# Kernel optimization log

Hardware: AMD Instinct MI355X
Metric: run time of the kernel (lower is better)

The kernel has to match this reference:

```python
import jax, jax.numpy as jnp
import numpy as np

B, S, D, H, E, TOPK = 8, 1024, 512, 2048, 8, 2


def setup_inputs() -> dict:
    key = jax.random.key(0)
    ks = jax.random.split(key, 7)
    scale = 0.02
    return {
        "x": jax.random.normal(ks[0], (B, S, D), jnp.float32),
        "gate_w": jax.random.normal(ks[1], (D, E), jnp.float32) * scale,
        "gate_b": jnp.zeros((E,), jnp.float32),
        "w1": jax.random.normal(ks[2], (E, D, H), jnp.float32) * scale,
        "b1": jnp.zeros((E, H), jnp.float32),
        "w2": jax.random.normal(ks[3], (E, H, D), jnp.float32) * scale,
        "b2": jnp.zeros((E, D), jnp.float32),
    }


def reference(x, gate_w, gate_b, w1, b1, w2, b2):
    # ---- MoE transformer MLP (fastmoe FMoETransformerMLP, NaiveGate) ----
    xt = x.reshape(-1, D)                       # [T, D], T = B*S tokens
    logits = xt @ gate_w + gate_b               # [T, E]
    top_val, top_idx = jax.lax.top_k(logits, TOPK)  # [T, k]
    score = jax.nn.softmax(top_val, axis=-1)    # softmax over the k selected logits

    y = jnp.zeros_like(xt)
    # Loop over the small fixed expert set; each token's combine weight for
    # expert e is the sum of its top-k scores routed to e (0 if not selected).
    for e in range(E):
        w_tok = jnp.sum(score * (top_idx == e), axis=-1)        # [T]
        h = jax.nn.gelu(xt @ w1[e] + b1[e], approximate=False)  # [T, H]
        y = y + w_tok[:, None] * (h @ w2[e] + b2[e])            # [T, D]

    y = y.reshape(B, S, D)
    # Outer model: log_softmax over seq of channel-summed features
    return jax.nn.log_softmax(jnp.sum(y, axis=2), axis=1)       # [B, S]
```

## Files before the change

### kernel.cpp

```cpp
#include <hip/hip_runtime.h>
#include <hip/hip_bf16.h>
#include <math.h>

#define T_TOK 8192
#define DIM   512
#define NEXP  8
#define HID   2048
#define NBAT  8
#define SEQ   1024

typedef short  short8 __attribute__((ext_vector_type(8)));
typedef float  f32x4  __attribute__((ext_vector_type(4)));

__device__ __forceinline__ unsigned short f2bf(float f) {
    union { float f; unsigned int u; } v; v.f = f;
    unsigned int u = v.u;
    unsigned int r = u + 0x7FFFu + ((u >> 16) & 1u);
    return (unsigned short)(r >> 16);
}

__device__ __forceinline__ float gelu_f(float v) {
    float v2 = v * v;
    float w = v * (-2.302344f - 0.102955f * v2);
    return v / (1.f + __builtin_amdgcn_exp2f(w));
}

__global__ void prep_gate_k(const float* __restrict__ w1, unsigned short* __restrict__ w1f,
                            const float* __restrict__ w2, const float* __restrict__ b2,
                            float* __restrict__ w2sum, float* __restrict__ b2sum,
                            int* __restrict__ counts,
                            const float* __restrict__ x, const float* __restrict__ gw,
                            const float* __restrict__ gb,
                            unsigned short* __restrict__ xb,
                            int* __restrict__ eidx, float* __restrict__ esc0,
                            float* __restrict__ esc1) {
    int bid = blockIdx.x;
    int tid = threadIdx.x;
    int wave = tid >> 6, lane = tid & 63;
    if (bid < 2048) {
        __shared__ unsigned short tile[64][68];
        int e = bid >> 8, r = bid & 255;
        int d0 = (r & 7) * 64, h0 = (r >> 3) * 64;
        const float* src = w1 + (size_t)e * DIM * HID;
        #pragma unroll
        for (int pass = 0; pass < 4; ++pass) {
            int dr = pass * 16 + (tid >> 4);
            int hc = (tid & 15) * 4;
            float4 v = *(const float4*)(src + (size_t)(d0 + dr) * HID + h0 + hc);
            tile[hc + 0][dr] = f2bf(v.x);
            tile[hc + 1][dr] = f2bf(v.y);
            tile[hc + 2][dr] = f2bf(v.z);
            tile[hc + 3][dr] = f2bf(v.w);
        }
        __syncthreads();
        int l = tid & 63, q = l >> 4, c = l & 15;
        int kk0 = (r & 7) * 2, g0 = (r >> 3) * 4;
        #pragma unroll
        for (int pi = 0; pi < 2; ++pi) {
            int sub = pi * 4 + wave;
            int kk2 = sub >> 2, g2 = sub & 3;
            const unsigned short* tp = &tile[g2 * 16 + c][kk2 * 32 + q * 8];
            ushort4 a = *(const ushort4*)(tp);
            ushort4 b = *(const ushort4*)(tp + 4);
            unsigned short* dst = w1f +
                ((size_t)(e * 128 + g0 + g2) * 16 + kk0 + kk2) * 512 + l * 8;
            *(ushort4*)(dst)     = a;
            *(ushort4*)(dst + 4) = b;
        }
    } else if (bid < 4096) {
        int t = (bid - 2048) * 4 + wave;
        const float* xp = x + (size_t)t * DIM;
        unsigned short* xbp = xb + (size_t)t * DIM;
        float acc[8] = {0, 0, 0, 0, 0, 0, 0, 0};
        #pragma unroll
        for (int it = 0; it < 8; ++it) {
            int d = it * 64 + lane;
            float xv = xp[d];
            xbp[d] = f2bf(xv);
            float4 g0 = *(const float4*)(gw + d * 8);
            float4 g1 = *(const float4*)(gw + d * 8 + 4);
            acc[0] += xv * g0.x; acc[1] += xv * g0.y; acc[2] += xv * g0.z; acc[3] += xv * g0.w;
            acc[4] += xv * g1.x; acc[5] += xv * g1.y; acc[6] += xv * g1.z; acc[7] += xv * g1.w;
        }
        #pragma unroll
        for (int e = 0; e < 8; ++e) {
            float s = acc[e];
            #pragma unroll
            for (int off = 32; off >= 1; off >>= 1) s += __shfl_xor(s, off);
            acc[e] = s + gb[e];
        }
        float v0 = -1e30f, v1 = -1e30f; int i0 = 0, i1 = 0;
        #pragma unroll
        for (int e = 0; e < 8; ++e) {
            float v = acc[e];
            if (v > v0) { v1 = v0; i1 = i0; v0 = v; i0 = e; }
            else if (v > v1) { v1 = v; i1 = e; }
        }
        float e1 = expf(v1 - v0);
        float inv = 1.f / (1.f + e1);
        if (lane == 0) {
            eidx[t] = i0 | (i1 << 4);
            esc0[t] = inv;
            esc1[t] = e1 * inv;
        }
    } else if (bid < 8192) {
        int row = (bid - 4096) * 4 + wave;
        const float* p = w2 + (size_t)row * DIM;
        float4 a = *(const float4*)(p + lane * 4);
        float4 b = *(const float4*)(p + 256 + lane * 4);
        float s = a.x + a.y + a.z + a.w + b.x + b.y + b.z + b.w;
        #pragma unroll
        for (int off = 32; off >= 1; off >>= 1) s += __shfl_xor(s, off);
        if (lane == 0) w2sum[row] = s;
    } else {
        if (tid < 8) counts[tid] = 0;
        for (int r = wave; r < NEXP; r += 4) {
            const float* p = b2 + (size_t)r * DIM;
            float s = 0.f;
            for (int i = lane; i < DIM; i += 64) s += p[i];
            #pragma unroll
            for (int off = 32; off >= 1; off >>= 1) s += __shfl_xor(s, off);
            if (lane == 0) b2sum[r] = s;
        }
    }
}

__global__ __launch_bounds__(1024) void route_k(
    const int* __restrict__ eidx, const float* __restrict__ esc0,
    const float* __restrict__ esc1, const float* __restrict__ b2sum,
    int* __restrict__ counts,
    int* __restrict__ ptok, float* __restrict__ pscore,
    float* __restrict__ s_partial) {
    int tid = threadIdx.x;
    int t = blockIdx.x * 1024 + tid;
    int wv = tid >> 6, lane = tid & 63;
    int pk = eidx[t];
    int i0 = pk & 0xf, i1 = (pk >> 4) & 0xf;
    float s0 = esc0[t], s1 = esc1[t];

    s_partial[t] = s0 * b2sum[i0] + s1 * b2sum[i1];

    __shared__ int waveCnt[16][8];
    __shared__ int waveBase[16][8];

    unsigned long long m0[8], m1[8];
    #pragma unroll
    for (int e = 0; e < 8; ++e) {
        m0[e] = __ballot(i0 == e);
        m1[e] = __ballot(i1 == e);
    }
    if (lane < 8) {
        int c = 0;
        #pragma unroll
        for (int e = 0; e < 8; ++e)
            if (lane == e) c = __popcll(m0[e]) + __popcll(m1[e]);
        waveCnt[wv][lane] = c;
    }
    __syncthreads();
    if (tid < 8) {
        int e = tid;
        int total = 0;
        #pragma unroll
        for (int w = 0; w < 16; ++w) total += waveCnt[w][e];
        int base = atomicAdd(&counts[e], total);
        int run = base;
        #pragma unroll
        for (int w = 0; w < 16; ++w) {
            waveBase[w][e] = run;
            run += waveCnt[w][e];
        }
    }
    __syncthreads();

    unsigned long long lt = (1ULL << lane) - 1ULL;
    int slot0 = 0, slot1 = 0;
    #pragma unroll
    for (int e = 0; e < 8; ++e) {
        if (i0 == e) slot0 = waveBase[wv][e] + __popcll(m0[e] & lt);
        if (i1 == e) slot1 = waveBase[wv][e] + __popcll(m0[e]) + __popcll(m1[e] & lt);
    }
    ptok[i0 * T_TOK + slot0] = t;  pscore[i0 * T_TOK + slot0] = s0;
    ptok[i1 * T_TOK + slot1] = t;  pscore[i1 * T_TOK + slot1] = s1;
}

#define GPTR(p) (const __attribute__((address_space(1))) void*)(p)
#define LPTR(p) (__attribute__((address_space(3))) void*)(p)

__global__ __launch_bounds__(256, 4) void moe_gemm_k(
    const unsigned short* __restrict__ xb, const unsigned short* __restrict__ w1f,
    const float* __restrict__ b1, const float* __restrict__ w2sum,
    const int* __restrict__ counts, const int* __restrict__ ptok,
    const float* __restrict__ pscore, float* __restrict__ s_partial) {

    int flat = blockIdx.x + (int)blockIdx.y * 135;
    int xcd = flat & 7;
    int s = flat >> 3;
    int bx = s >> 1;
    int hBase = (xcd * 2 + (s & 1)) * 128;

    int e = 8, rowBase = 0, accT = 0;
    #pragma unroll
    for (int i = 0; i < 8; ++i) {
        int nt = (counts[i] + 127) >> 7;
        if (e == 8 && bx < accT + nt) { e = i; rowBase = (bx - accT) * 128; }
        accT += nt;
    }
    if (e == 8) return;
    int n_e = counts[e];

    __shared__ unsigned short A_s[2][128 * 32];
    __shared__ int   tokLds[128];
    __shared__ float scoreLds[128];

    int tid = threadIdx.x;
    int wave = tid >> 6, lane = tid & 63;

    if (tid < 128) {
        int r = rowBase + tid;
        bool valid = r < n_e;
        tokLds[tid]   = valid ? ptok[e * T_TOK + r]   : 0;
        scoreLds[tid] = valid ? pscore[e * T_TOK + r] : 0.f;
    }
    __syncthreads();

    const unsigned short* gA[2];
    int lo[2];
    #pragma unroll
    for (int i = 0; i < 2; ++i) {
        int c = (i * 4 + wave) * 64 + lane;
        int stripe = c >> 3, slot = c & 7;
        int sp = slot ^ (stripe & 7);
        int row = 2 * stripe + (sp >> 2);
        int j = (sp & 3) * 8;
        gA[i] = xb + (size_t)tokLds[row] * DIM + j;
        lo[i] = c * 8;
    }

    int wm = wave >> 1, wn = wave & 1;
    int quad = lane >> 4, col = lane & 15;

    f32x4 acc[4][4];
    #pragma unroll
    for (int m = 0; m < 4; ++m)
        #pragma unroll
        for (int n = 0; n < 4; ++n)
            acc[m][n] = (f32x4){0.f, 0.f, 0.f, 0.f};

    int rslot = (((col & 1) << 2) | quad) ^ ((col >> 1) & 7);
    int aOff = (wm * 32 + (col >> 1)) * 64 + rslot * 8;

    const unsigned short* bp = w1f +
        (size_t)(e * 128 + (hBase >> 4) + wn * 4) * 8192 + lane * 8;
    short8 bf[4];

    #pragma unroll
    for (int n = 0; n < 4; ++n) bf[n] = *(const short8*)(bp + n * 8192);
    #pragma unroll
    for (int i = 0; i < 2; ++i)
        __builtin_amdgcn_global_load_lds(GPTR(gA[i]), LPTR(&A_s[0][lo[i]]), 16, 0, 0);
    #pragma unroll
    for (int i = 0; i < 2; ++i)
        __builtin_amdgcn_global_load_lds(GPTR(gA[i] + 32), LPTR(&A_s[1][lo[i]]), 16, 0, 0);

    #pragma unroll
    for (int kk = 0; kk < 16; ++kk) {
        const int cur = kk & 1;
        if (kk == 0) { asm volatile("s_waitcnt vmcnt(2)" ::: "memory"); }
        else         { asm volatile("s_waitcnt vmcnt(6)" ::: "memory"); }
        __builtin_amdgcn_s_barrier();

        short8 af[4];
        const unsigned short* aB = &A_s[cur][aOff];
        #pragma unroll
        for (int m = 0; m < 4; ++m) af[m] = *(const short8*)(aB + m * 512);
        asm volatile("s_waitcnt lgkmcnt(0)" ::: "memory");
        __builtin_amdgcn_s_barrier();

        if (kk < 14) {
            int ko = (kk + 2) * 32;
            #pragma unroll
            for (int i = 0; i < 2; ++i)
                __builtin_amdgcn_global_load_lds(GPTR(gA[i] + ko), LPTR(&A_s[cur][lo[i]]), 16, 0, 0);
        }
        __builtin_amdgcn_sched_barrier(0);

        __builtin_amdgcn_s_setprio(1);
        #pragma unroll
        for (int m = 0; m < 4; ++m)
            #pragma unroll
            for (int n = 0; n < 4; ++n)
                acc[m][n] = __builtin_amdgcn_mfma_f32_16x16x32_bf16(af[m], bf[n], acc[m][n], 0, 0, 0);
        __builtin_amdgcn_s_setprio(0);

        if (kk < 15) {
            #pragma unroll
            for (int n = 0; n < 4; ++n)
                bf[n] = *(const short8*)(bp + n * 8192 + (kk + 1) * 512);
        }
    }

    const float* b1e = b1 + e * HID;
    const float* w2e = w2sum + e * HID;
    float bias[4], wsum[4];
    #pragma unroll
    for (int n = 0; n < 4; ++n) {
        int h = hBase + wn * 64 + n * 16 + col;
        bias[n] = b1e[h];
        wsum[n] = w2e[h];
    }
    #pragma unroll
    for (int m = 0; m < 4; ++m) {
        float rp0 = 0.f, rp1 = 0.f, rp2 = 0.f, rp3 = 0.f;
        #pragma unroll
        for (int n = 0; n < 4; ++n) {
            rp0 += gelu_f(acc[m][n][0] + bias[n]) * wsum[n];
            rp1 += gelu_f(acc[m][n][1] + bias[n]) * wsum[n];
            rp2 += gelu_f(acc[m][n][2] + bias[n]) * wsum[n];
            rp3 += gelu_f(acc[m][n][3] + bias[n]) * wsum[n];
        }
        #pragma unroll
        for (int off = 8; off >= 1; off >>= 1) {
            rp0 += __shfl_xor(rp0, off);
            rp1 += __shfl_xor(rp1, off);
            rp2 += __shfl_xor(rp2, off);
            rp3 += __shfl_xor(rp3, off);
        }
        if (col < 4) {
            float mine = (col == 0) ? rp0 : (col == 1) ? rp1 : (col == 2) ? rp2 : rp3;
            int rl = wm * 64 + m * 16 + quad * 4 + col;
            int r = rowBase + rl;
            if (r < n_e)
                atomicAdd(&s_partial[tokLds[rl]], scoreLds[rl] * mine);
        }
    }
}

__global__ void lsm_k(const float* __restrict__ s, float* __restrict__ out) {
    int b = blockIdx.x, tid = threadIdx.x;
    int wave = tid >> 6, lane = tid & 63;
    __shared__ float red[4];
    const float* sp = s + (size_t)b * SEQ;
    float v[4];
    #pragma unroll
    for (int i = 0; i < 4; ++i) v[i] = sp[tid + i * 256];
    float m = fmaxf(fmaxf(v[0], v[1]), fmaxf(v[2], v[3]));
    #pragma unroll
    for (int off = 32; off >= 1; off >>= 1) m = fmaxf(m, __shfl_xor(m, off));
    if (lane == 0) red[wave] = m;
    __syncthreads();
    m = fmaxf(fmaxf(red[0], red[1]), fmaxf(red[2], red[3]));
    __syncthreads();
    float t = 0.f;
    #pragma unroll
    for (int i = 0; i < 4; ++i) t += expf(v[i] - m);
    #pragma unroll
    for (int off = 32; off >= 1; off >>= 1) t += __shfl_xor(t, off);
    if (lane == 0) red[wave] = t;
    __syncthreads();
    t = red[0] + red[1] + red[2] + red[3];
    float L = m + logf(t);
    #pragma unroll
    for (int i = 0; i < 4; ++i) out[(size_t)b * SEQ + tid + i * 256] = v[i] - L;
}

extern "C" void kernel_launch(void* const* d_in, const int* in_sizes, int n_in,
                              void* d_out, int out_size, void* d_ws, size_t ws_size,
                              hipStream_t stream) {
    const float* x  = (const float*)d_in[0];
    const float* gw = (const float*)d_in[1];
    const float* gb = (const float*)d_in[2];
    const float* w1 = (const float*)d_in[3];
    const float* b1 = (const float*)d_in[4];
    const float* w2 = (const float*)d_in[5];
    const float* b2 = (const float*)d_in[6];
    float* out = (float*)d_out;

    char* ws = (char*)d_ws;
    int*   counts    = (int*)  (ws + 0);
    float* b2sum     = (float*)(ws + 1280);
    float* s_partial = (float*)(ws + 1536);
    float* w2sum     = (float*)(ws + 34304);
    int*   ptok      = (int*)  (ws + 99840);
    float* pscore    = (float*)(ws + 361984);
    int*   eidx      = (int*)  (ws + 624128);
    float* esc0      = (float*)(ws + 656896);
    float* esc1      = (float*)(ws + 689664);
    unsigned short* xb  = (unsigned short*)(ws + 722432);
    unsigned short* w1f = (unsigned short*)(ws + 9111040);

    prep_gate_k<<<8193, 256, 0, stream>>>(w1, w1f, w2, b2, w2sum, b2sum, counts,
                                          x, gw, gb, xb, eidx, esc0, esc1);
    route_k<<<NEXP, 1024, 0, stream>>>(eidx, esc0, esc1, b2sum, counts, ptok, pscore, s_partial);
    moe_gemm_k<<<dim3(135, 16), 256, 0, stream>>>(xb, w1f, b1, w2sum, counts, ptok, pscore, s_partial);
    lsm_k<<<NBAT, 256, 0, stream>>>(s_partial, out);
}
```

Before: 184.2 us.

## Double the K-chunk per stage to 64 and halve pipeline iterations

Doubles the A-tile LDS stage from 32 to 64 K-columns, so each barrier-synchronised iteration covers two MFMA K-steps and the loop drops from 16 to 8 iterations. It also changes the gathered-token load layout to row-major with an XOR swizzle, and retunes the vmcnt waits to match the larger in-flight load count. The aim is to cut the per-iteration barrier and wait overhead. In exchange it uses more LDS, which may lower occupancy, and the hand-tuned vmcnt values must count outstanding loads exactly or stale data is read.

```diff
diff --git a/kernel.cpp b/kernel.cpp
--- a/kernel.cpp
+++ b/kernel.cpp
@@ -208,7 +208,7 @@
     if (e == 8) return;
     int n_e = counts[e];
 
-    __shared__ unsigned short A_s[2][128 * 32];
+    __shared__ unsigned short A_s[2][128 * 64];
     __shared__ int   tokLds[128];
     __shared__ float scoreLds[128];
 
@@ -223,17 +223,13 @@
     }
     __syncthreads();
 
-    const unsigned short* gA[2];
-    int lo[2];
-    #pragma unroll
-    for (int i = 0; i < 2; ++i) {
-        int c = (i * 4 + wave) * 64 + lane;
-        int stripe = c >> 3, slot = c & 7;
-        int sp = slot ^ (stripe & 7);
-        int row = 2 * stripe + (sp >> 2);
-        int j = (sp & 3) * 8;
-        gA[i] = xb + (size_t)tokLds[row] * DIM + j;
-        lo[i] = c * 8;
+    unsigned gAo[4];
+    #pragma unroll
+    for (int i = 0; i < 4; ++i) {
+        int c = i * 256 + tid;
+        int row = c >> 3, pos = c & 7;
+        int j = (pos ^ (row & 7)) * 8;
+        gAo[i] = (unsigned)tokLds[row] * DIM + j;
     }
 
     int wm = wave >> 1, wn = wave & 1;
@@ -246,41 +242,47 @@
         for (int n = 0; n < 4; ++n)
             acc[m][n] = (f32x4){0.f, 0.f, 0.f, 0.f};
 
-    int rslot = (((col & 1) << 2) | quad) ^ ((col >> 1) & 7);
-    int aOff = (wm * 32 + (col >> 1)) * 64 + rslot * 8;
+    int aOff0 = (wm * 64 + col) * 64 + ((((0 << 2) | quad) ^ (col & 7)) * 8);
+    int aOff1 = (wm * 64 + col) * 64 + ((((1 << 2) | quad) ^ (col & 7)) * 8);
 
     const unsigned short* bp = w1f +
         (size_t)(e * 128 + (hBase >> 4) + wn * 4) * 8192 + lane * 8;
     short8 bf[4];
 
     #pragma unroll
+    for (int i = 0; i < 4; ++i)
+        __builtin_amdgcn_global_load_lds(GPTR(xb + gAo[i]), LPTR(&A_s[0][i * 2048 + tid * 8]), 16, 0, 0);
+    __builtin_amdgcn_sched_barrier(0);
+    #pragma unroll
+    for (int i = 0; i < 4; ++i)
+        __builtin_amdgcn_global_load_lds(GPTR(xb + gAo[i] + 64), LPTR(&A_s[1][i * 2048 + tid * 8]), 16, 0, 0);
+    __builtin_amdgcn_sched_barrier(0);
+    #pragma unroll
     for (int n = 0; n < 4; ++n) bf[n] = *(const short8*)(bp + n * 8192);
-    #pragma unroll
-    for (int i = 0; i < 2; ++i)
-        __builtin_amdgcn_global_load_lds(GPTR(gA[i]), LPTR(&A_s[0][lo[i]]), 16, 0, 0);
-    #pragma unroll
-    for (int i = 0; i < 2; ++i)
-        __builtin_amdgcn_global_load_lds(GPTR(gA[i] + 32), LPTR(&A_s[1][lo[i]]), 16, 0, 0);
-
-    #pragma unroll
-    for (int kk = 0; kk < 16; ++kk) {
+    __builtin_amdgcn_sched_barrier(0);
+
+    #pragma unroll
+    for (int kk = 0; kk < 8; ++kk) {
         const int cur = kk & 1;
-        if (kk == 0) { asm volatile("s_waitcnt vmcnt(2)" ::: "memory"); }
-        else         { asm volatile("s_waitcnt vmcnt(6)" ::: "memory"); }
+        if (kk == 0)                 { asm volatile("s_waitcnt vmcnt(8)"  ::: "memory"); }
+        else if (kk == 1 || kk == 7) { asm volatile("s_waitcnt vmcnt(16)" ::: "memory"); }
+        else                         { asm volatile("s_waitcnt vmcnt(20)" ::: "memory"); }
         __builtin_amdgcn_s_barrier();
 
-        short8 af[4];
-        const unsigned short* aB = &A_s[cur][aOff];
-        #pragma unroll
-        for (int m = 0; m < 4; ++m) af[m] = *(const short8*)(aB + m * 512);
+        short8 af0[4], af1[4];
+        const unsigned short* aB = &A_s[cur][0];
+        #pragma unroll
+        for (int m = 0; m < 4; ++m) af0[m] = *(const short8*)(aB + aOff0 + m * 1024);
+        #pragma unroll
+        for (int m = 0; m < 4; ++m) af1[m] = *(const short8*)(aB + aOff1 + m * 1024);
         asm volatile("s_waitcnt lgkmcnt(0)" ::: "memory");
         __builtin_amdgcn_s_barrier();
 
-        if (kk < 14) {
-            int ko = (kk + 2) * 32;
-            #pragma unroll
-            for (int i = 0; i < 2; ++i)
-                __builtin_amdgcn_global_load_lds(GPTR(gA[i] + ko), LPTR(&A_s[cur][lo[i]]), 16, 0, 0);
+        if (kk < 6) {
+            int ko = (kk + 2) * 64;
+            #pragma unroll
+            for (int i = 0; i < 4; ++i)
+                __builtin_amdgcn_global_load_lds(GPTR(xb + gAo[i] + ko), LPTR(&A_s[cur][i * 2048 + tid * 8]), 16, 0, 0);
         }
         __builtin_amdgcn_sched_barrier(0);
 
@@ -289,13 +291,25 @@
         for (int m = 0; m < 4; ++m)
             #pragma unroll
             for (int n = 0; n < 4; ++n)
-                acc[m][n] = __builtin_amdgcn_mfma_f32_16x16x32_bf16(af[m], bf[n], acc[m][n], 0, 0, 0);
+                acc[m][n] = __builtin_amdgcn_mfma_f32_16x16x32_bf16(af0[m], bf[n], acc[m][n], 0, 0, 0);
         __builtin_amdgcn_s_setprio(0);
 
-        if (kk < 15) {
+        #pragma unroll
+        for (int n = 0; n < 4; ++n)
+            bf[n] = *(const short8*)(bp + (2 * kk + 1) * 512 + n * 8192);
+
+        __builtin_amdgcn_s_setprio(1);
+        #pragma unroll
+        for (int m = 0; m < 4; ++m)
             #pragma unroll
             for (int n = 0; n < 4; ++n)
-                bf[n] = *(const short8*)(bp + n * 8192 + (kk + 1) * 512);
+                acc[m][n] = __builtin_amdgcn_mfma_f32_16x16x32_bf16(af1[m], bf[n], acc[m][n], 0, 0, 0);
+        __builtin_amdgcn_s_setprio(0);
+
+        if (kk < 7) {
+            #pragma unroll
+            for (int n = 0; n < 4; ++n)
+                bf[n] = *(const short8*)(bp + (2 * kk + 2) * 512 + n * 8192);
         }
     }
 
```

Result: slower. 222.1 us (+20.6%).
